# Kernel optimization log

Measured on AMD Instinct MI355X. Metric: run time of the kernel, lower is better.

## Reference

```python
import jax, jax.numpy as jnp
import numpy as np

B, Q, C, H, W, CH = 16, 1024, 256, 32, 32, 8  # batch, queries, dim, grid, conv hidden


def setup_inputs() -> dict:
    key = jax.random.key(0)
    ks = jax.random.split(key, 8)
    return {
        "queries": jax.random.normal(ks[0], (B, Q, C), jnp.float32),
        "keys": jax.random.normal(ks[1], (B, H, W, C), jnp.float32),
        "pos": jax.random.randint(ks[2], (B, Q, 2), 0, H, dtype=jnp.int32),
        "rel_bias": jax.random.normal(ks[3], (2 * H - 1, 2 * W - 1), jnp.float32) * 0.02,
        "conv1_weight": jax.random.normal(ks[4], (CH, 1, 3, 3), jnp.float32) * 0.1,
        "conv1_bias": jnp.zeros((CH,), jnp.float32),
        "conv2_weight": jax.random.normal(ks[5], (1, CH, 3, 3), jnp.float32) * 0.1,
        "conv2_bias": jnp.zeros((1,), jnp.float32),
    }


def reference(queries, keys, pos, rel_bias, conv1_weight, conv1_bias, conv2_weight, conv2_bias):
    Bq, Qn, Cd = queries.shape
    _, Hh, Ww, _ = keys.shape
    # fused relative-grid attention scores: [B,Q,H,W]
    scores = jnp.einsum('bqc,bhwc->bqhw', queries, keys) / jnp.sqrt(jnp.float32(Cd))
    dh = jnp.arange(Hh)[None, None, :] - pos[..., 0][..., None] + (Hh - 1)  # [B,Q,H]
    dw = jnp.arange(Ww)[None, None, :] - pos[..., 1][..., None] + (Ww - 1)  # [B,Q,W]
    bias = rel_bias[dh[..., :, None], dw[..., None, :]]                     # [B,Q,H,W]
    attn = jax.nn.softmax((scores + bias).reshape(Bq, Qn, Hh * Ww), axis=-1)
    attn = attn.reshape(Bq, Qn, Hh, Ww)
    # residual conv block on each (1,H,W) attention map
    x = attn.reshape(Bq * Qn, 1, Hh, Ww)
    dn = ('NCHW', 'OIHW', 'NCHW')
    h = jax.lax.conv_general_dilated(x, conv1_weight, (1, 1), 'SAME', dimension_numbers=dn)
    h = jax.nn.relu(h + conv1_bias[None, :, None, None])
    h = jax.lax.conv_general_dilated(h, conv2_weight, (1, 1), 'SAME', dimension_numbers=dn)
    h = h + conv2_bias[None, :, None, None]
    return (x + h).reshape(Bq, Qn, Hh, Ww)
```

## Files before the change

### kernel.cpp

```cpp
#include <hip/hip_runtime.h>

typedef _Float16 h2 __attribute__((ext_vector_type(2)));
typedef _Float16 h8 __attribute__((ext_vector_type(8)));
typedef float f32x4 __attribute__((ext_vector_type(4)));

#define B_  16
#define Q_  1024
#define C_  256
#define HW_ 1024
#define TQA 64
#define NTA 512
#define QLD 264
#define BT  256
#define IPB 4
#define XRB 80
#define XIMGB (34 * XRB)
#define HRB 576

__device__ __forceinline__ h2 u2h(unsigned u) { return __builtin_bit_cast(h2, u); }
__device__ __forceinline__ unsigned h2u(h2 h) { return __builtin_bit_cast(unsigned, h); }

__device__ __forceinline__ h2 pkfma(h2 a, h2 b, h2 c) {
#if __has_builtin(__builtin_elementwise_fma)
    return __builtin_elementwise_fma(a, b, c);
#else
    return a * b + c;
#endif
}
__device__ __forceinline__ h2 pkmax0(h2 a) {
#if __has_builtin(__builtin_elementwise_max)
    return __builtin_elementwise_max(a, (h2)(_Float16)0.f);
#else
    h2 r;
    r[0] = a[0] > (_Float16)0.f ? a[0] : (_Float16)0.f;
    r[1] = a[1] > (_Float16)0.f ? a[1] : (_Float16)0.f;
    return r;
#endif
}

__global__ void cvt_keys_f16(const float* __restrict__ src,
                             _Float16* __restrict__ dst, int n8) {
    int i = blockIdx.x * blockDim.x + threadIdx.x;
    if (i >= n8) return;
    const float4* s = (const float4*)src;
    float4 a = s[2 * i], b = s[2 * i + 1];
    h8 v;
    v[0] = (_Float16)a.x; v[1] = (_Float16)a.y; v[2] = (_Float16)a.z; v[3] = (_Float16)a.w;
    v[4] = (_Float16)b.x; v[5] = (_Float16)b.y; v[6] = (_Float16)b.z; v[7] = (_Float16)b.w;
    *(h8*)(dst + (size_t)i * 8) = v;
}

__global__ void pack_weights(const float* __restrict__ w1, const float* __restrict__ b1,
                             const float* __restrict__ w2, const float* __restrict__ b2,
                             unsigned* __restrict__ wpk) {
    int t = threadIdx.x;
    if (t < 24) {
        int ch = t / 3, dy = t - ch * 3;
        h2 v = {(_Float16)w1[ch * 9 + dy * 3 + 0], (_Float16)w1[ch * 9 + dy * 3 + 1]};
        wpk[t] = h2u(v);
    } else if (t < 48) {
        int i = t - 24; int ch = i / 3, dy = i - ch * 3;
        h2 v = {(_Float16)w1[ch * 9 + dy * 3 + 2], (_Float16)0.f};
        wpk[t] = h2u(v);
    } else if (t < 56) {
        wpk[t] = __builtin_bit_cast(unsigned, b1[t - 48]);
    } else if (t < 92) {
        int i = t - 56; int t9 = i >> 2, c2 = i & 3;
        h2 v = {(_Float16)w2[(2 * c2) * 9 + t9], (_Float16)w2[(2 * c2 + 1) * 9 + t9]};
        wpk[t] = h2u(v);
    } else if (t == 92) {
        wpk[t] = __builtin_bit_cast(unsigned, b2[0]);
    } else if (t >= 96 && t < 168) {
        int i = t - 96; int tap = i >> 3, ch = i & 7;
        _Float16 w = (_Float16)w1[ch * 9 + tap];
        h2 v = {w, w};
        wpk[t] = h2u(v);
    } else if (t >= 168 && t < 176) {
        _Float16 b = (_Float16)b1[t - 168];
        h2 v = {b, b};
        wpk[t] = h2u(v);
    }
}

__global__ __launch_bounds__(NTA, 2) void attn_kernel(
    const float* __restrict__ queries, const _Float16* __restrict__ keysh,
    const int* __restrict__ pos, const float* __restrict__ rel_bias,
    _Float16* __restrict__ xmapg)
{
    __shared__ _Float16 q_lds[TQA * QLD];
    __shared__ _Float16 bias_lds[63 * 64];
    __shared__ float red_max[8][TQA];
    __shared__ float red_sum[8][TQA];
    __shared__ int2  pos_lds[TQA];

    const int tid = threadIdx.x;
    const int bid = blockIdx.x;
    const int swz = (bid & 7) * 32 + (bid >> 3);
    const int batch = swz >> 4;
    const int tile  = swz & 15;

    {
        const float4* qsrc = (const float4*)(queries + (size_t)(batch * Q_ + tile * TQA) * C_);
        #pragma unroll
        for (int i = 0; i < 8; ++i) {
            int e4 = i * NTA + tid;
            float4 v = qsrc[e4];
            int row = e4 >> 6, col4 = e4 & 63;
            _Float16* d = &q_lds[row * QLD + col4 * 4];
            d[0] = (_Float16)v.x; d[1] = (_Float16)v.y;
            d[2] = (_Float16)v.z; d[3] = (_Float16)v.w;
        }
        for (int idx = tid; idx < 63 * 63; idx += NTA) {
            int r = idx / 63;
            bias_lds[r * 64 + (idx - r * 63)] = (_Float16)rel_bias[idx];
        }
        if (tid < TQA)
            pos_lds[tid] = ((const int2*)pos)[batch * Q_ + tile * TQA + tid];
    }
    __syncthreads();

    const int lane = tid & 63;
    const int wv   = tid >> 6;
    const int kgrp = (lane >> 4) * 8;
    const int l15  = lane & 15;
    const int rowbase = (lane >> 4) << 2;

    f32x4 acc[4][8];
    #pragma unroll
    for (int mt = 0; mt < 4; ++mt)
        #pragma unroll
        for (int f = 0; f < 8; ++f) acc[mt][f] = f32x4{0.f, 0.f, 0.f, 0.f};

    const _Float16* kb = keysh + (size_t)batch * (HW_ * C_)
                       + (size_t)(wv * 128 + l15) * C_ + kgrp;
    #pragma unroll
    for (int ks = 0; ks < 8; ++ks) {
        h8 a[4];
        #pragma unroll
        for (int mt = 0; mt < 4; ++mt)
            a[mt] = *(const h8*)&q_lds[(mt * 16 + l15) * QLD + ks * 32 + kgrp];
        #pragma unroll
        for (int f = 0; f < 8; ++f) {
            h8 bfr = *(const h8*)(kb + f * (16 * C_) + ks * 32);
            #pragma unroll
            for (int mt = 0; mt < 4; ++mt)
                acc[mt][f] = __builtin_amdgcn_mfma_f32_16x16x32_f16(a[mt], bfr, acc[mt][f], 0, 0, 0);
        }
    }

    int p0r[4][4], p1r[4][4];
    #pragma unroll
    for (int mt = 0; mt < 4; ++mt)
        #pragma unroll
        for (int r = 0; r < 4; ++r) {
            int2 pp = pos_lds[mt * 16 + rowbase + r];
            p0r[mt][r] = pp.x; p1r[mt][r] = pp.y;
        }

    float mrow[4][4];
    #pragma unroll
    for (int mt = 0; mt < 4; ++mt)
        #pragma unroll
        for (int r = 0; r < 4; ++r) mrow[mt][r] = -3e38f;

    #pragma unroll
    for (int f = 0; f < 8; ++f) {
        int col = wv * 128 + f * 16 + l15;
        int hh = col >> 5, ww = col & 31;
        #pragma unroll
        for (int mt = 0; mt < 4; ++mt)
            #pragma unroll
            for (int r = 0; r < 4; ++r) {
                float s = acc[mt][f][r] * 0.0625f
                        + (float)bias_lds[(hh - p0r[mt][r] + 31) * 64 + (ww - p1r[mt][r] + 31)];
                acc[mt][f][r] = s;
                mrow[mt][r] = fmaxf(mrow[mt][r], s);
            }
    }
    #pragma unroll
    for (int mt = 0; mt < 4; ++mt)
        #pragma unroll
        for (int r = 0; r < 4; ++r) {
            float m = mrow[mt][r];
            m = fmaxf(m, __shfl_xor(m, 1, 64));
            m = fmaxf(m, __shfl_xor(m, 2, 64));
            m = fmaxf(m, __shfl_xor(m, 4, 64));
            m = fmaxf(m, __shfl_xor(m, 8, 64));
            mrow[mt][r] = m;
        }
    if (l15 == 0) {
        #pragma unroll
        for (int mt = 0; mt < 4; ++mt)
            #pragma unroll
            for (int r = 0; r < 4; ++r)
                red_max[wv][mt * 16 + rowbase + r] = mrow[mt][r];
    }
    __syncthreads();

    float sm[4][4];
    #pragma unroll
    for (int mt = 0; mt < 4; ++mt)
        #pragma unroll
        for (int r = 0; r < 4; ++r) {
            float m = red_max[0][mt * 16 + rowbase + r];
            #pragma unroll
            for (int w = 1; w < 8; ++w) m = fmaxf(m, red_max[w][mt * 16 + rowbase + r]);
            mrow[mt][r] = m;
            sm[mt][r] = 0.f;
        }

    #pragma unroll
    for (int f = 0; f < 8; ++f) {
        #pragma unroll
        for (int mt = 0; mt < 4; ++mt)
            #pragma unroll
            for (int r = 0; r < 4; ++r) {
                float e = __expf(acc[mt][f][r] - mrow[mt][r]);
                acc[mt][f][r] = e;
                sm[mt][r] += e;
            }
    }
    #pragma unroll
    for (int mt = 0; mt < 4; ++mt)
        #pragma unroll
        for (int r = 0; r < 4; ++r) {
            float s = sm[mt][r];
            s += __shfl_xor(s, 1, 64);
            s += __shfl_xor(s, 2, 64);
            s += __shfl_xor(s, 4, 64);
            s += __shfl_xor(s, 8, 64);
            sm[mt][r] = s;
        }
    if (l15 == 0) {
        #pragma unroll
        for (int mt = 0; mt < 4; ++mt)
            #pragma unroll
            for (int r = 0; r < 4; ++r)
                red_sum[wv][mt * 16 + rowbase + r] = sm[mt][r];
    }
    __syncthreads();

    _Float16* xg = xmapg + (size_t)(batch * Q_ + tile * TQA) * HW_;
    #pragma unroll
    for (int mt = 0; mt < 4; ++mt) {
        float sinv[4];
        #pragma unroll
        for (int r = 0; r < 4; ++r) {
            float S = red_sum[0][mt * 16 + rowbase + r];
            #pragma unroll
            for (int w = 1; w < 8; ++w) S += red_sum[w][mt * 16 + rowbase + r];
            sinv[r] = 1.0f / S;
        }
        #pragma unroll
        for (int f = 0; f < 8; ++f) {
            int col = wv * 128 + f * 16 + l15;
            #pragma unroll
            for (int r = 0; r < 4; ++r)
                xg[(size_t)(mt * 16 + rowbase + r) * HW_ + col]
                    = (_Float16)(acc[mt][f][r] * sinv[r]);
        }
    }
}

__global__ __launch_bounds__(BT, 4) void conv_kernel(
    const _Float16* __restrict__ xmapg, const unsigned* __restrict__ wpk,
    float* __restrict__ out)
{
    __shared__ __align__(16) char xall[16 + IPB * XIMGB];
    __shared__ __align__(16) char Hb[34 * HRB];
    __shared__ unsigned wsh[176];

    const int tid = threadIdx.x;
    const int bid = blockIdx.x;
    const int swz = (bid & 7) * 512 + (bid >> 3);
    const size_t img0 = (size_t)swz * IPB;

    {
        const uint4 z = uint4{0u, 0u, 0u, 0u};
        uint4* xz = (uint4*)xall;
        for (int i = tid; i < (int)sizeof(xall) / 16; i += BT) xz[i] = z;
        uint4* hz = (uint4*)Hb;
        for (int i = tid; i < (int)sizeof(Hb) / 16; i += BT) hz[i] = z;
    }
    if (tid < 176) wsh[tid] = wpk[tid];
    __syncthreads();

    #pragma unroll
    for (int i = 0; i < 2; ++i) {
        int c = i * BT + tid;
        int im = c >> 7, cc = c & 127, r = cc >> 2, q = cc & 3;
        uint4 v = *(const uint4*)(xmapg + img0 * HW_ + (size_t)im * HW_ + cc * 8);
        *(uint4*)(xall + 16 + im * XIMGB + (r + 1) * XRB + q * 16) = v;
    }

    const int m4 = tid & 7;
    const int y  = tid >> 3;
    const int x0 = m4 << 2;

    const char* const xrow0 = xall + 16 + y * XRB + x0 * 2;
    char* const hwr = Hb + (y + 1) * HRB + m4 * 16;
    const char* const hrd = Hb + y * HRB + m4 * 16;

    __syncthreads();

    #pragma unroll 1
    for (int img = 0; img < IPB; ++img) {
        const char* xi = xrow0 + img * XIMGB;

        unsigned Pm[3], A0[3], Pc[3], A1[3], Pe[3];
        #pragma unroll
        for (int dy = 0; dy < 3; ++dy) {
            unsigned em = *(const unsigned*)(xi + dy * XRB - 4);
            uint2 a01   = *(const uint2*)(xi + dy * XRB);
            unsigned e4 = *(const unsigned*)(xi + dy * XRB + 8);
            A0[dy] = a01.x; A1[dy] = a01.y;
            Pm[dy] = __builtin_amdgcn_alignbit(a01.x, em, 16);
            Pc[dy] = __builtin_amdgcn_alignbit(a01.y, a01.x, 16);
            Pe[dy] = __builtin_amdgcn_alignbit(e4, a01.y, 16);
        }

        unsigned hvw[4][4];
        #pragma unroll
        for (int p2 = 0; p2 < 2; ++p2) {
            h2 accp[8];
            #pragma unroll
            for (int ch = 0; ch < 8; ++ch)
                accp[ch] = u2h(wsh[168 + ch]);
            #pragma unroll
            for (int dy = 0; dy < 3; ++dy) {
                const unsigned W0 = p2 ? Pc[dy] : Pm[dy];
                const unsigned W1 = p2 ? A1[dy] : A0[dy];
                const unsigned W2 = p2 ? Pe[dy] : Pc[dy];
                #pragma unroll
                for (int ch = 0; ch < 8; ++ch) {
                    accp[ch] = pkfma(u2h(W0), u2h(wsh[96 + (dy * 3 + 0) * 8 + ch]), accp[ch]);
                    accp[ch] = pkfma(u2h(W1), u2h(wsh[96 + (dy * 3 + 1) * 8 + ch]), accp[ch]);
                    accp[ch] = pkfma(u2h(W2), u2h(wsh[96 + (dy * 3 + 2) * 8 + ch]), accp[ch]);
                }
            }
            #pragma unroll
            for (int w = 0; w < 4; ++w) {
                unsigned a = h2u(pkmax0(accp[2 * w]));
                unsigned b = h2u(pkmax0(accp[2 * w + 1]));
                hvw[2 * p2 + 0][w] = (a & 0xffffu) | (b << 16);
                hvw[2 * p2 + 1][w] = (a >> 16) | (b & 0xffff0000u);
            }
        }

        __syncthreads();

        {
            *(uint4*)(hwr + 144) = uint4{hvw[0][0], hvw[0][1], hvw[0][2], hvw[0][3]};
            *(uint4*)(hwr + 288) = uint4{hvw[1][0], hvw[1][1], hvw[1][2], hvw[1][3]};
            *(uint4*)(hwr + 432) = uint4{hvw[2][0], hvw[2][1], hvw[2][2], hvw[2][3]};
            *(uint4*)(hwr + 16)  = uint4{hvw[3][0], hvw[3][1], hvw[3][2], hvw[3][3]};
        }
        __syncthreads();

        h2 a2p[4];
        #pragma unroll
        for (int j = 0; j < 4; ++j) a2p[j] = u2h(0u);
        #pragma unroll
        for (int dy = 0; dy < 3; ++dy) {
            const char* rb = hrd + dy * HRB;
            uint4 Hv[6];
            Hv[0] = *(const uint4*)(rb + 0);
            Hv[1] = *(const uint4*)(rb + 144);
            Hv[2] = *(const uint4*)(rb + 288);
            Hv[3] = *(const uint4*)(rb + 432);
            Hv[4] = *(const uint4*)(rb + 16);
            Hv[5] = *(const uint4*)(rb + 160);
            #pragma unroll
            for (int dx = 0; dx < 3; ++dx) {
                const int tt = dy * 3 + dx;
                const h2 w0 = u2h(wsh[56 + tt * 4 + 0]);
                const h2 w1 = u2h(wsh[56 + tt * 4 + 1]);
                const h2 w2 = u2h(wsh[56 + tt * 4 + 2]);
                const h2 w3 = u2h(wsh[56 + tt * 4 + 3]);
                #pragma unroll
                for (int j = 0; j < 4; ++j) {
                    const uint4 uu = Hv[j + dx];
                    a2p[j] = pkfma(u2h(uu.x), w0, a2p[j]);
                    a2p[j] = pkfma(u2h(uu.y), w1, a2p[j]);
                    a2p[j] = pkfma(u2h(uu.z), w2, a2p[j]);
                    a2p[j] = pkfma(u2h(uu.w), w3, a2p[j]);
                }
            }
        }
        {
            const float b2r = __builtin_bit_cast(float, wsh[92]);
            h2 lo = u2h(A0[1]), hi = u2h(A1[1]);
            float4 o;
            o.x = (float)lo[0] + (float)a2p[0][0] + (float)a2p[0][1] + b2r;
            o.y = (float)lo[1] + (float)a2p[1][0] + (float)a2p[1][1] + b2r;
            o.z = (float)hi[0] + (float)a2p[2][0] + (float)a2p[2][1] + b2r;
            o.w = (float)hi[1] + (float)a2p[3][0] + (float)a2p[3][1] + b2r;
            *(float4*)(out + (img0 + img) * HW_ + y * 32 + x0) = o;
        }
    }
}

extern "C" void kernel_launch(void* const* d_in, const int* in_sizes, int n_in,
                              void* d_out, int out_size, void* d_ws, size_t ws_size,
                              hipStream_t stream) {
    const float* queries  = (const float*)d_in[0];
    const float* keys     = (const float*)d_in[1];
    const int*   pos      = (const int*)d_in[2];
    const float* rel_bias = (const float*)d_in[3];
    const float* w1       = (const float*)d_in[4];
    const float* b1       = (const float*)d_in[5];
    const float* w2       = (const float*)d_in[6];
    const float* b2       = (const float*)d_in[7];
    float* out = (float*)d_out;

    unsigned*  wpk   = (unsigned*)d_ws;
    _Float16*  keysh = (_Float16*)((char*)d_ws + 4096);
    _Float16*  xmapg = (_Float16*)((char*)d_ws + 4096 + 8388608);

    const int n8 = (B_ * HW_ * C_) / 8;
    pack_weights<<<dim3(1), dim3(192), 0, stream>>>(w1, b1, w2, b2, wpk);
    cvt_keys_f16<<<dim3(n8 / 256), dim3(256), 0, stream>>>(keys, keysh, n8);
    attn_kernel<<<dim3(B_ * (Q_ / TQA)), dim3(NTA), 0, stream>>>(
        queries, keysh, pos, rel_bias, xmapg);
    conv_kernel<<<dim3((B_ * Q_) / IPB), dim3(BT), 0, stream>>>(xmapg, wpk, out);
}
```

Before: 108.7 us.

## Fold weight packing into key conversion and merge conv1 column-pair loops

Removes the separate single-block pack_weights launch by having block 0 of the key-conversion kernel write the packed weights, and drops the unused wpk entries 0-55. The conv kernel's first convolution now computes both column pairs in one loop so each weight loaded from shared memory is reused twice, and launch bounds rise to 5 blocks per SM. Fusing the launches saves launch overhead, while the higher occupancy target and the doubled accumulators both add register pressure and could cause spills.

```diff
diff --git a/kernel.cpp b/kernel.cpp
--- a/kernel.cpp
+++ b/kernel.cpp
@@ -39,8 +39,30 @@
 }
 
 __global__ void cvt_keys_f16(const float* __restrict__ src,
-                             _Float16* __restrict__ dst, int n8) {
+                             _Float16* __restrict__ dst, int n8,
+                             const float* __restrict__ w1, const float* __restrict__ b1,
+                             const float* __restrict__ w2, const float* __restrict__ b2,
+                             unsigned* __restrict__ wpk) {
     int i = blockIdx.x * blockDim.x + threadIdx.x;
+    if (blockIdx.x == 0) {
+        int t = threadIdx.x;
+        if (t >= 56 && t < 92) {
+            int k = t - 56; int t9 = k >> 2, c2 = k & 3;
+            h2 v = {(_Float16)w2[(2 * c2) * 9 + t9], (_Float16)w2[(2 * c2 + 1) * 9 + t9]};
+            wpk[t] = h2u(v);
+        } else if (t == 92) {
+            wpk[t] = __builtin_bit_cast(unsigned, b2[0]);
+        } else if (t >= 96 && t < 168) {
+            int k = t - 96; int tap = k >> 3, ch = k & 7;
+            _Float16 w = (_Float16)w1[ch * 9 + tap];
+            h2 v = {w, w};
+            wpk[t] = h2u(v);
+        } else if (t >= 168 && t < 176) {
+            _Float16 b = (_Float16)b1[t - 168];
+            h2 v = {b, b};
+            wpk[t] = h2u(v);
+        }
+    }
     if (i >= n8) return;
     const float4* s = (const float4*)src;
     float4 a = s[2 * i], b = s[2 * i + 1];
@@ -48,38 +70,6 @@
     v[0] = (_Float16)a.x; v[1] = (_Float16)a.y; v[2] = (_Float16)a.z; v[3] = (_Float16)a.w;
     v[4] = (_Float16)b.x; v[5] = (_Float16)b.y; v[6] = (_Float16)b.z; v[7] = (_Float16)b.w;
     *(h8*)(dst + (size_t)i * 8) = v;
-}
-
-__global__ void pack_weights(const float* __restrict__ w1, const float* __restrict__ b1,
-                             const float* __restrict__ w2, const float* __restrict__ b2,
-                             unsigned* __restrict__ wpk) {
-    int t = threadIdx.x;
-    if (t < 24) {
-        int ch = t / 3, dy = t - ch * 3;
-        h2 v = {(_Float16)w1[ch * 9 + dy * 3 + 0], (_Float16)w1[ch * 9 + dy * 3 + 1]};
-        wpk[t] = h2u(v);
-    } else if (t < 48) {
-        int i = t - 24; int ch = i / 3, dy = i - ch * 3;
-        h2 v = {(_Float16)w1[ch * 9 + dy * 3 + 2], (_Float16)0.f};
-        wpk[t] = h2u(v);
-    } else if (t < 56) {
-        wpk[t] = __builtin_bit_cast(unsigned, b1[t - 48]);
-    } else if (t < 92) {
-        int i = t - 56; int t9 = i >> 2, c2 = i & 3;
-        h2 v = {(_Float16)w2[(2 * c2) * 9 + t9], (_Float16)w2[(2 * c2 + 1) * 9 + t9]};
-        wpk[t] = h2u(v);
-    } else if (t == 92) {
-        wpk[t] = __builtin_bit_cast(unsigned, b2[0]);
-    } else if (t >= 96 && t < 168) {
-        int i = t - 96; int tap = i >> 3, ch = i & 7;
-        _Float16 w = (_Float16)w1[ch * 9 + tap];
-        h2 v = {w, w};
-        wpk[t] = h2u(v);
-    } else if (t >= 168 && t < 176) {
-        _Float16 b = (_Float16)b1[t - 168];
-        h2 v = {b, b};
-        wpk[t] = h2u(v);
-    }
 }
 
 __global__ __launch_bounds__(NTA, 2) void attn_kernel(
@@ -262,7 +252,7 @@
     }
 }
 
-__global__ __launch_bounds__(BT, 4) void conv_kernel(
+__global__ __launch_bounds__(BT, 5) void conv_kernel(
     const _Float16* __restrict__ xmapg, const unsigned* __restrict__ wpk,
     float* __restrict__ out)
 {
@@ -319,32 +309,38 @@
             Pe[dy] = __builtin_amdgcn_alignbit(e4, a01.y, 16);
         }
 
+        h2 acc0[8], acc1[8];
+        #pragma unroll
+        for (int ch = 0; ch < 8; ++ch) {
+            h2 b = u2h(wsh[168 + ch]);
+            acc0[ch] = b; acc1[ch] = b;
+        }
+        #pragma unroll
+        for (int dy = 0; dy < 3; ++dy) {
+            #pragma unroll
+            for (int ch = 0; ch < 8; ++ch) {
+                const h2 wt0 = u2h(wsh[96 + (dy * 3 + 0) * 8 + ch]);
+                const h2 wt1 = u2h(wsh[96 + (dy * 3 + 1) * 8 + ch]);
+                const h2 wt2 = u2h(wsh[96 + (dy * 3 + 2) * 8 + ch]);
+                acc0[ch] = pkfma(u2h(Pm[dy]), wt0, acc0[ch]);
+                acc0[ch] = pkfma(u2h(A0[dy]), wt1, acc0[ch]);
+                acc0[ch] = pkfma(u2h(Pc[dy]), wt2, acc0[ch]);
+                acc1[ch] = pkfma(u2h(Pc[dy]), wt0, acc1[ch]);
+                acc1[ch] = pkfma(u2h(A1[dy]), wt1, acc1[ch]);
+                acc1[ch] = pkfma(u2h(Pe[dy]), wt2, acc1[ch]);
+            }
+        }
         unsigned hvw[4][4];
         #pragma unroll
-        for (int p2 = 0; p2 < 2; ++p2) {
-            h2 accp[8];
-            #pragma unroll
-            for (int ch = 0; ch < 8; ++ch)
-                accp[ch] = u2h(wsh[168 + ch]);
-            #pragma unroll
-            for (int dy = 0; dy < 3; ++dy) {
-                const unsigned W0 = p2 ? Pc[dy] : Pm[dy];
-                const unsigned W1 = p2 ? A1[dy] : A0[dy];
-                const unsigned W2 = p2 ? Pe[dy] : Pc[dy];
-                #pragma unroll
-                for (int ch = 0; ch < 8; ++ch) {
-                    accp[ch] = pkfma(u2h(W0), u2h(wsh[96 + (dy * 3 + 0) * 8 + ch]), accp[ch]);
-                    accp[ch] = pkfma(u2h(W1), u2h(wsh[96 + (dy * 3 + 1) * 8 + ch]), accp[ch]);
-                    accp[ch] = pkfma(u2h(W2), u2h(wsh[96 + (dy * 3 + 2) * 8 + ch]), accp[ch]);
-                }
-            }
-            #pragma unroll
-            for (int w = 0; w < 4; ++w) {
-                unsigned a = h2u(pkmax0(accp[2 * w]));
-                unsigned b = h2u(pkmax0(accp[2 * w + 1]));
-                hvw[2 * p2 + 0][w] = (a & 0xffffu) | (b << 16);
-                hvw[2 * p2 + 1][w] = (a >> 16) | (b & 0xffff0000u);
-            }
+        for (int w = 0; w < 4; ++w) {
+            unsigned a0 = h2u(pkmax0(acc0[2 * w]));
+            unsigned b0 = h2u(pkmax0(acc0[2 * w + 1]));
+            hvw[0][w] = (a0 & 0xffffu) | (b0 << 16);
+            hvw[1][w] = (a0 >> 16) | (b0 & 0xffff0000u);
+            unsigned a1 = h2u(pkmax0(acc1[2 * w]));
+            unsigned b1w = h2u(pkmax0(acc1[2 * w + 1]));
+            hvw[2][w] = (a1 & 0xffffu) | (b1w << 16);
+            hvw[3][w] = (a1 >> 16) | (b1w & 0xffff0000u);
         }
 
         __syncthreads();
@@ -418,8 +414,8 @@
     _Float16*  xmapg = (_Float16*)((char*)d_ws + 4096 + 8388608);
 
     const int n8 = (B_ * HW_ * C_) / 8;
-    pack_weights<<<dim3(1), dim3(192), 0, stream>>>(w1, b1, w2, b2, wpk);
-    cvt_keys_f16<<<dim3(n8 / 256), dim3(256), 0, stream>>>(keys, keysh, n8);
+    cvt_keys_f16<<<dim3(n8 / 256), dim3(256), 0, stream>>>(keys, keysh, n8,
+                                                           w1, b1, w2, b2, wpk);
     attn_kernel<<<dim3(B_ * (Q_ / TQA)), dim3(NTA), 0, stream>>>(
         queries, keysh, pos, rel_bias, xmapg);
     conv_kernel<<<dim3((B_ * Q_) / IPB), dim3(BT), 0, stream>>>(xmapg, wpk, out);
```

Result: faster. 106.2 us (-2.3%).
